# Optimization experiments

Hardware: AMD Instinct MI355X
Metric: run time of the kernel (lower is better)

## Reference

```python
import jax, jax.numpy as jnp
import numpy as np

T_IN, T_TGT, B = 192, 192, 128
XDIM, CH, H, Z, OUT = 64, 2, 512, 128, 64
XIN = XDIM * CH


def _gru_cell(h, x_proj, Whh, bhh):
    # torch GRU gate order: r, z, n
    hp = h @ Whh.T + bhh
    xr, xz, xn = jnp.split(x_proj, 3, axis=-1)
    hr, hz, hn = jnp.split(hp, 3, axis=-1)
    r = jax.nn.sigmoid(xr + hr)
    zg = jax.nn.sigmoid(xz + hz)
    n = jnp.tanh(xn + r * hn)
    return (1.0 - zg) * n + zg * h


def _run_gru(xs, h0, Wih, bih, Whh, bhh):
    xp = xs @ Wih.T + bih  # [T, B, 3H] precomputed input projections
    def step(h, xpt):
        h2 = _gru_cell(h, xpt, Whh, bhh)
        return h2, h2
    hT, outs = jax.lax.scan(step, h0, xp)
    return outs, hT


def setup_inputs() -> dict:
    key = jax.random.key(0)
    ks = jax.random.split(key, 40)
    p = lambda i, shape: jax.random.normal(ks[i], shape, jnp.float32) * 0.05
    inp = {
        "x": jax.random.normal(ks[0], (T_IN, B, XIN), jnp.float32),
        "target": jax.random.normal(ks[1], (T_TGT, B, XDIM), jnp.float32),
        "eps_z": jax.random.normal(ks[2], (2, B, Z), jnp.float32),
        "eps_y": jax.random.normal(ks[3], (T_TGT, B, OUT), jnp.float32),
        # phi_x MLP
        "W_phi1": p(4, (H, XIN)), "b_phi1": jnp.zeros((H,), jnp.float32),
        "W_phi2": p(5, (H, H)), "b_phi2": jnp.zeros((H,), jnp.float32),
        # encoder bidirectional GRU
        "Wih_ef": p(6, (3 * H, H)), "bih_ef": jnp.zeros((3 * H,), jnp.float32),
        "Whh_ef": p(7, (3 * H, H)), "bhh_ef": jnp.zeros((3 * H,), jnp.float32),
        "Wih_eb": p(8, (3 * H, H)), "bih_eb": jnp.zeros((3 * H,), jnp.float32),
        "Whh_eb": p(9, (3 * H, H)), "bhh_eb": jnp.zeros((3 * H,), jnp.float32),
        # latent heads
        "W_mean": p(10, (Z, H)), "b_mean": jnp.zeros((Z,), jnp.float32),
        "W_std": p(11, (Z, H)), "b_std": jnp.zeros((Z,), jnp.float32),
        # first decoder hidden
        "W_fh": p(12, (H, 2 * Z)), "b_fh": jnp.zeros((H,), jnp.float32),
        # decoder GRU, input size H + 2Z (order: [z_expanded, state])
        "Wih_d": p(13, (3 * H, 2 * Z + H)), "bih_d": jnp.zeros((3 * H,), jnp.float32),
        "Whh_d": p(14, (3 * H, H)), "bhh_d": jnp.zeros((3 * H,), jnp.float32),
        # decoder output heads
        "W_dm": p(15, (OUT, H)), "b_dm": jnp.zeros((OUT,), jnp.float32),
        "W_ds": p(16, (OUT, H)), "b_ds": jnp.zeros((OUT,), jnp.float32),
        "epoch": 0,
    }
    return inp


def reference(x, target, eps_z, eps_y,
              W_phi1, b_phi1, W_phi2, b_phi2,
              Wih_ef, bih_ef, Whh_ef, bhh_ef,
              Wih_eb, bih_eb, Whh_eb, bhh_eb,
              W_mean, b_mean, W_std, b_std,
              W_fh, b_fh, Wih_d, bih_d, Whh_d, bhh_d,
              W_dm, b_dm, W_ds, b_ds, epoch):
    Bsz, h_dim = x.shape[1], W_phi1.shape[0]
    two_z = W_fh.shape[1]
    # phi_x
    phi = jax.nn.relu(jax.nn.relu(x @ W_phi1.T + b_phi1) @ W_phi2.T + b_phi2)
    h0 = jnp.zeros((Bsz, h_dim), phi.dtype)
    # bidirectional encoder: final hidden of each direction
    _, hf = _run_gru(phi, h0, Wih_ef, bih_ef, Whh_ef, bhh_ef)
    _, hb = _run_gru(phi[::-1], h0, Wih_eb, bih_eb, Whh_eb, bhh_eb)
    enc_h = jnp.stack([hf, hb])  # [2, B, H]
    latent_mean = enc_h @ W_mean.T + b_mean
    latent_std = jax.nn.softplus(enc_h @ W_std.T + b_std)
    z = eps_z * latent_std + latent_mean  # [2, B, Z]
    z_exp = jnp.concatenate([z[0], z[1]], axis=1)  # [B, 2Z]
    dec_h0 = jnp.tanh(z_exp @ W_fh.T + b_fh)
    # decoder input = concat([z_exp, state]); split Wih_d columns accordingly
    W_z, W_s = Wih_d[:, :two_z], Wih_d[:, two_z:]
    z_proj = z_exp @ W_z.T + bih_d  # constant part of input projection

    def step(carry, eps_t):
        h, s = carry  # s is previous decoder_out (zeros at t=0)
        xp = z_proj + s @ W_s.T
        h2 = _gru_cell(h, xp, Whh_d, bhh_d)
        m = jax.nn.softplus(h2 @ W_dm.T + b_dm)
        st = jax.nn.softplus(h2 @ W_ds.T + b_ds)
        pred = eps_t * st + m
        return (h2, h2), (pred, m, st)

    s0 = jnp.zeros_like(dec_h0)
    _, (preds, means, stds) = jax.lax.scan(step, (dec_h0, s0), eps_y)
    return latent_mean, latent_std, z, preds, means, stds
```

## Files before the change

### kernel.cpp

```cpp
#include <hip/hip_runtime.h>
#include <stdint.h>

typedef __attribute__((ext_vector_type(4))) float    f32x4;
typedef __attribute__((ext_vector_type(8))) short    s16x8;
typedef __attribute__((ext_vector_type(4))) short    s16x4;
typedef __attribute__((ext_vector_type(4))) unsigned u32x4;
typedef __attribute__((ext_vector_type(8))) __bf16   bf16x8;

#define DEV __device__ __forceinline__

DEV float b2f(short h) {
  unsigned u = ((unsigned)(unsigned short)h) << 16;
  return __builtin_bit_cast(float, u);
}
DEV short f2b(float f) {
  unsigned u = __builtin_bit_cast(unsigned, f);
  u = (u + 0x7FFFu + ((u >> 16) & 1u)) >> 16;
  return (short)u;
}
DEV float fsig(float x) { return 1.0f / (1.0f + __expf(-x)); }
DEV float ftanh(float x) {
  x = fminf(fmaxf(x, -15.0f), 15.0f);
  float e = __expf(2.0f * x);
  return (e - 1.0f) / (e + 1.0f);
}
DEV float fsp(float x) { return (x > 20.0f) ? x : __logf(1.0f + __expf(x)); }

DEV f32x4 MFMA(s16x8 a, s16x8 b, f32x4 c) {
  return __builtin_amdgcn_mfma_f32_16x16x32_bf16(
      __builtin_bit_cast(bf16x8, a), __builtin_bit_cast(bf16x8, b), c, 0, 0, 0);
}
DEV void gload16(const void* g, void* l) {
  __builtin_amdgcn_global_load_lds(
      (const __attribute__((address_space(1))) unsigned*)g,
      (__attribute__((address_space(3))) unsigned*)l, 16, 0, 0);
}

DEV s16x8 ld16c(const short* p) {
  s16x8 r;
  asm volatile("global_load_dwordx4 %0, %1, off sc0 sc1" : "=v"(r) : "v"(p) : "memory");
  return r;
}
DEV void st8c(short* p, s16x4 v) {
  asm volatile("global_store_dwordx2 %0, %1, off sc0 sc1" :: "v"(p), "v"(v) : "memory");
}
DEV void stflagc(unsigned* p, unsigned v) {
  asm volatile("global_store_dword %0, %1, off sc0 sc1" :: "v"(p), "v"(v) : "memory");
}
DEV void poll8c(const unsigned* f, unsigned tgt) {
  unsigned gd = 0;
  for (;;) {
    u32x4 a, b;
    asm volatile("global_load_dwordx4 %0, %2, off sc0 sc1\n\t"
                 "global_load_dwordx4 %1, %2, off offset:16 sc0 sc1\n\t"
                 "s_waitcnt vmcnt(0)"
                 : "=v"(a), "=v"(b) : "v"(f) : "memory");
    unsigned m = a[0];
    m = a[1] < m ? a[1] : m; m = a[2] < m ? a[2] : m; m = a[3] < m ? a[3] : m;
    m = b[0] < m ? b[0] : m; m = b[1] < m ? b[1] : m;
    m = b[2] < m ? b[2] : m; m = b[3] < m ? b[3] : m;
    if (m >= tgt) return;
    if (++gd > (1u << 18)) return;
  }
}

__global__ void k_initf(unsigned* __restrict__ f) {
  stflagc(f + threadIdx.x * 2, 0u);
  stflagc(f + threadIdx.x * 2 + 1, 0u);
}

__global__ void k_f2b(const float* __restrict__ s, short* __restrict__ d, int n) {
  int i = (blockIdx.x * 256 + threadIdx.x) * 4;
  if (i >= n) return;
  float4 v = *(const float4*)(s + i);
  s16x4 o; o[0] = f2b(v.x); o[1] = f2b(v.y); o[2] = f2b(v.z); o[3] = f2b(v.w);
  *(s16x4*)(d + i) = o;
}
__global__ void k_f2bs(const float* __restrict__ s, short* __restrict__ d,
                       int cols, int sstr, int soff, int total) {
  int i = (blockIdx.x * 256 + threadIdx.x) * 4;
  if (i >= total) return;
  int r = i / cols, c = i - r * cols;
  float4 v = *(const float4*)(s + (size_t)r * sstr + soff + c);
  s16x4 o; o[0] = f2b(v.x); o[1] = f2b(v.y); o[2] = f2b(v.z); o[3] = f2b(v.w);
  *(s16x4*)(d + i) = o;
}
__global__ void k_build_dec(const float* __restrict__ Whh, const float* __restrict__ Wih,
                            short* __restrict__ out) {
  int i = (blockIdx.x * 256 + threadIdx.x) * 4;
  if (i >= 1048576) return;
  int r = i >> 9, c = i & 511;
  float4 v;
  if (r < 1024) {
    float4 a = *(const float4*)(Whh + (size_t)r * 512 + c);
    float4 b = *(const float4*)(Wih + (size_t)r * 768 + 256 + c);
    v = make_float4(a.x + b.x, a.y + b.y, a.z + b.z, a.w + b.w);
  } else if (r < 1536) {
    v = *(const float4*)(Wih + (size_t)r * 768 + 256 + c);
  } else {
    v = *(const float4*)(Whh + (size_t)(r - 512) * 512 + c);
  }
  s16x4 o; o[0] = f2b(v.x); o[1] = f2b(v.y); o[2] = f2b(v.z); o[3] = f2b(v.w);
  *(s16x4*)(out + i) = o;
}

template <int EPI>
__global__ __launch_bounds__(256) void kgemm(
    const short* __restrict__ A, const short* __restrict__ W,
    const float* __restrict__ bias, float* __restrict__ outF,
    short* __restrict__ outB, int M, int N, int K) {
  __shared__ short lA[8192];
  __shared__ short lB[8192];
  const int tid = threadIdx.x, lane = tid & 63, wid = tid >> 6;
  const int l15 = lane & 15, lq = lane >> 4;
  const int m0 = blockIdx.x * 128, n0 = blockIdx.y * 128;
  const int wr2 = wid >> 1, wc2 = wid & 1;
  const f32x4 vz = {0.f, 0.f, 0.f, 0.f};
  f32x4 acc[4][4];
#pragma unroll
  for (int i = 0; i < 4; ++i)
#pragma unroll
    for (int j = 0; j < 4; ++j) acc[i][j] = vz;
  const int Kb = K * 2;
  const int nkt = K >> 6;
  const int srow = lane >> 3, sk = (lane & 7) * 16;
  const char* gA = (const char*)A;
  const char* gW = (const char*)W;
  for (int kt = 0; kt < nkt; ++kt) {
    __syncthreads();
#pragma unroll
    for (int i = 0; i < 4; ++i) {
      const int c = wid * 4 + i;
      gload16(gA + (size_t)(m0 + c * 8 + srow) * Kb + kt * 128 + sk, (char*)lA + c * 1024);
      gload16(gW + (size_t)(n0 + c * 8 + srow) * Kb + kt * 128 + sk, (char*)lB + c * 1024);
    }
    __syncthreads();
#pragma unroll
    for (int kc = 0; kc < 2; ++kc) {
      s16x8 af[4], bf[4];
#pragma unroll
      for (int mt = 0; mt < 4; ++mt)
        af[mt] = *(const s16x8*)((const char*)lA + (wr2 * 64 + mt * 16 + l15) * 128 + kc * 64 + lq * 16);
#pragma unroll
      for (int nt = 0; nt < 4; ++nt)
        bf[nt] = *(const s16x8*)((const char*)lB + (wc2 * 64 + nt * 16 + l15) * 128 + kc * 64 + lq * 16);
#pragma unroll
      for (int mt = 0; mt < 4; ++mt)
#pragma unroll
        for (int nt = 0; nt < 4; ++nt)
          acc[mt][nt] = MFMA(af[mt], bf[nt], acc[mt][nt]);
    }
  }
#pragma unroll
  for (int mt = 0; mt < 4; ++mt) {
#pragma unroll
    for (int nt = 0; nt < 4; ++nt) {
      const int col = n0 + wc2 * 64 + nt * 16 + l15;
      const int rl = wr2 * 64 + mt * 16 + lq * 4;
      const int row = m0 + rl;
      const float bv = bias ? bias[col] : 0.f;
      if (EPI == 0) {
#pragma unroll
        for (int d = 0; d < 4; ++d) outF[(size_t)(row + d) * N + col] = acc[mt][nt][d] + bv;
      } else if (EPI == 1) {
#pragma unroll
        for (int d = 0; d < 4; ++d) {
          float v = acc[mt][nt][d] + bv;
          v = v > 0.f ? v : 0.f;
          outB[(size_t)(row + d) * N + col] = f2b(v);
        }
      } else if (EPI == 3) {
#pragma unroll
        for (int d = 0; d < 4; ++d) {
          float v = ftanh(acc[mt][nt][d] + bv);
          outF[(size_t)(row + d) * N + col] = v;
          outB[(size_t)(row + d) * N + col] = f2b(v);
        }
      } else {
#pragma unroll
        for (int d = 0; d < 4; ++d)
          outB[(size_t)(row + d) * N + col] = f2b(acc[mt][nt][d] + bv);
      }
    }
  }
}

DEV void enc_xp_load(const short* xp, int tt, int J0, int lq, int b,
                     short xv[3][4]) {
  const short* xr = xp + (size_t)(tt * 128 + b) * 1536;
#pragma unroll
  for (int g = 0; g < 3; ++g)
#pragma unroll
    for (int d = 0; d < 4; ++d)
      xv[g][d] = xr[g * 512 + J0 + lq * 4 + d];
}

__global__ __launch_bounds__(256, 1) void enc_scan(
    const short* __restrict__ xpTf, const short* __restrict__ xpTb,
    const short* __restrict__ Whf, const short* __restrict__ Whb,
    const float* __restrict__ bhf, const float* __restrict__ bhb,
    short* __restrict__ hB, short* __restrict__ ench,
    unsigned* __restrict__ flags) {
  const int tid = threadIdx.x, lane = tid & 63, wid = tid >> 6;
  const int l15 = lane & 15, lq = lane >> 4;
  const int w = blockIdx.x;
  const int gru = w >> 6, rr = w & 63, bg = rr >> 3, cw = rr & 7;
  const int J0 = (cw * 4 + wid) * 16, b0 = bg * 16;
  const int b = b0 + l15;
  const short* Wg = gru ? Whb : Whf;
  const float* bb = gru ? bhb : bhf;
  const short* xpT = gru ? xpTb : xpTf;
  short* hBg = hB + (size_t)gru * 131072;
  unsigned* gfl = flags + (gru * 8 + bg) * 16;
  const f32x4 vz = {0.f, 0.f, 0.f, 0.f};

  s16x8 wfr[3][16];
#pragma unroll
  for (int g = 0; g < 3; ++g) {
    const short* wrp = Wg + (size_t)(g * 512 + J0 + l15) * 512 + lq * 8;
#pragma unroll
    for (int kc = 0; kc < 16; ++kc) wfr[g][kc] = *(const s16x8*)(wrp + kc * 32);
  }
  float bi[3][4];
#pragma unroll
  for (int g = 0; g < 3; ++g)
#pragma unroll
    for (int d = 0; d < 4; ++d) bi[g][d] = bb[g * 512 + J0 + lq * 4 + d];
  float hpv[4];
#pragma unroll
  for (int d = 0; d < 4; ++d) hpv[d] = 0.f;

  short xpv[3][4];
  enc_xp_load(xpT, gru ? 191 : 0, J0, lq, b, xpv);
  const int chb = J0 + lq * 4;

  {
    s16x4 pk;
#pragma unroll
    for (int d = 0; d < 4; ++d) {
      float rg = fsig(b2f(xpv[0][d]) + bi[0][d]);
      float zg = fsig(b2f(xpv[1][d]) + bi[1][d]);
      float nn = ftanh(b2f(xpv[2][d]) + rg * bi[2][d]);
      float hv = (1.f - zg) * nn;
      hpv[d] = hv;
      pk[d] = f2b(hv);
    }
    st8c(hBg + (((size_t)((chb >> 3) * 128 + b)) << 3) + (chb & 7), pk);
    asm volatile("s_waitcnt vmcnt(0)" ::: "memory");
    __syncthreads();
    if (tid == 0) stflagc(gfl + cw, 1u);
    enc_xp_load(xpT, gru ? 190 : 1, J0, lq, b, xpv);
  }

  for (int t = 1; t < 192; ++t) {
    poll8c(gfl, (unsigned)t);
    s16x8 hb[16];
    const short* hsrc = hBg + ((t + 1) & 1) * 65536;
#pragma unroll
    for (int kc = 0; kc < 16; ++kc)
      hb[kc] = ld16c(hsrc + ((size_t)((kc * 4 + lq) * 128 + b) << 3));
    asm volatile("s_waitcnt vmcnt(0)" ::: "memory");
    __builtin_amdgcn_sched_barrier(0);
    f32x4 acc[3];
#pragma unroll
    for (int g = 0; g < 3; ++g) acc[g] = vz;
#pragma unroll
    for (int kc = 0; kc < 16; ++kc)
#pragma unroll
      for (int g = 0; g < 3; ++g) acc[g] = MFMA(wfr[g][kc], hb[kc], acc[g]);
    short* hdst = hBg + (t & 1) * 65536;
    s16x4 pk;
#pragma unroll
    for (int d = 0; d < 4; ++d) {
      float rg = fsig(b2f(xpv[0][d]) + acc[0][d] + bi[0][d]);
      float zg = fsig(b2f(xpv[1][d]) + acc[1][d] + bi[1][d]);
      float nn = ftanh(b2f(xpv[2][d]) + rg * (acc[2][d] + bi[2][d]));
      float hv = (1.f - zg) * nn + zg * hpv[d];
      hpv[d] = hv;
      pk[d] = f2b(hv);
    }
    st8c(hdst + (((size_t)((chb >> 3) * 128 + b)) << 3) + (chb & 7), pk);
    if (t == 191) *(s16x4*)(ench + (size_t)gru * 65536 + (size_t)b * 512 + chb) = pk;
    asm volatile("s_waitcnt vmcnt(0)" ::: "memory");
    __syncthreads();
    if (tid == 0) stflagc(gfl + cw, (unsigned)(t + 1));
    if (t < 191) {
      const int tp = t + 1;
      enc_xp_load(xpT, gru ? (191 - tp) : tp, J0, lq, b, xpv);
    }
  }
}

__global__ __launch_bounds__(256, 1) void dec_scan(
    const short* __restrict__ zpR, const short* __restrict__ Wd,
    const float* __restrict__ bhd, const float* __restrict__ pre0,
    const float* __restrict__ h0f, short* __restrict__ hB,
    short* __restrict__ Hs, unsigned* __restrict__ flags) {
  const int tid = threadIdx.x, lane = tid & 63, wid = tid >> 6;
  const int l15 = lane & 15, lq = lane >> 4;
  const int w = blockIdx.x;
  const int bg = w >> 3, m = w & 7;
  unsigned* gfl = flags + 256 + bg * 16;
  const int J0 = (m * 4 + wid) * 16, b0 = bg * 16;
  const int b = b0 + l15;
  const f32x4 vz = {0.f, 0.f, 0.f, 0.f};

  s16x8 wfr[4][16];
#pragma unroll
  for (int g = 0; g < 4; ++g) {
    const short* wrp = Wd + (size_t)(g * 512 + J0 + l15) * 512 + lq * 8;
#pragma unroll
    for (int kc = 0; kc < 16; ++kc) wfr[g][kc] = *(const s16x8*)(wrp + kc * 32);
  }
  float bi[3][4];
#pragma unroll
  for (int g = 0; g < 3; ++g)
#pragma unroll
    for (int d = 0; d < 4; ++d) bi[g][d] = bhd[g * 512 + J0 + lq * 4 + d];
  short zpv[3][4];
#pragma unroll
  for (int g = 0; g < 3; ++g)
#pragma unroll
    for (int d = 0; d < 4; ++d)
      zpv[g][d] = zpR[(size_t)b * 1536 + g * 512 + J0 + lq * 4 + d];
  float hpv[4];
#pragma unroll
  for (int d = 0; d < 4; ++d) hpv[d] = h0f[(size_t)b * 512 + J0 + lq * 4 + d];
  const int chb = J0 + lq * 4;

  {
    s16x4 pk;
#pragma unroll
    for (int d = 0; d < 4; ++d) {
      float p0 = pre0[(size_t)b * 1536 + 0 * 512 + J0 + lq * 4 + d];
      float p1 = pre0[(size_t)b * 1536 + 1 * 512 + J0 + lq * 4 + d];
      float p2 = pre0[(size_t)b * 1536 + 2 * 512 + J0 + lq * 4 + d];
      float rg = fsig(b2f(zpv[0][d]) + p0);
      float zg = fsig(b2f(zpv[1][d]) + p1);
      float nn = ftanh(b2f(zpv[2][d]) + rg * p2);
      float hv = (1.f - zg) * nn + zg * hpv[d];
      hpv[d] = hv;
      pk[d] = f2b(hv);
    }
    st8c(hB + (((size_t)((chb >> 3) * 128 + b)) << 3) + (chb & 7), pk);
    asm volatile("s_waitcnt vmcnt(0)" ::: "memory");
    __syncthreads();
    if (tid == 0) stflagc(gfl + m, 1u);
    *(s16x4*)(Hs + (size_t)b * 512 + chb) = pk;
  }

  for (int t = 1; t < 192; ++t) {
    poll8c(gfl, (unsigned)t);
    s16x8 hb[16];
    const short* hsrc = hB + ((t + 1) & 1) * 65536;
#pragma unroll
    for (int kc = 0; kc < 16; ++kc)
      hb[kc] = ld16c(hsrc + ((size_t)((kc * 4 + lq) * 128 + b) << 3));
    asm volatile("s_waitcnt vmcnt(0)" ::: "memory");
    __builtin_amdgcn_sched_barrier(0);
    f32x4 acc[4];
#pragma unroll
    for (int g = 0; g < 4; ++g) acc[g] = vz;
#pragma unroll
    for (int kc = 0; kc < 16; ++kc)
#pragma unroll
      for (int g = 0; g < 4; ++g) acc[g] = MFMA(wfr[g][kc], hb[kc], acc[g]);
    short* hdst = hB + (t & 1) * 65536;
    s16x4 pk;
#pragma unroll
    for (int d = 0; d < 4; ++d) {
      float rg = fsig(b2f(zpv[0][d]) + acc[0][d] + bi[0][d]);
      float zg = fsig(b2f(zpv[1][d]) + acc[1][d] + bi[1][d]);
      float nn = ftanh(b2f(zpv[2][d]) + acc[2][d] + rg * (acc[3][d] + bi[2][d]));
      float hv = (1.f - zg) * nn + zg * hpv[d];
      hpv[d] = hv;
      pk[d] = f2b(hv);
    }
    st8c(hdst + (((size_t)((chb >> 3) * 128 + b)) << 3) + (chb & 7), pk);
    asm volatile("s_waitcnt vmcnt(0)" ::: "memory");
    __syncthreads();
    if (tid == 0) stflagc(gfl + m, (unsigned)(t + 1));
    *(s16x4*)(Hs + (size_t)(t * 128 + b) * 512 + chb) = pk;
  }
}

__global__ void k_latent(const float* __restrict__ tmp, const float* __restrict__ b_mean,
                         const float* __restrict__ b_std, const float* __restrict__ eps_z,
                         float* __restrict__ out, short* __restrict__ zexp) {
  int i = blockIdx.x * 256 + threadIdx.x;
  if (i >= 32768) return;
  int c = i & 127, b = (i >> 7) & 127, g = i >> 14;
  float mp = tmp[(size_t)(g * 128 + b) * 256 + c] + b_mean[c];
  float sp = fsp(tmp[(size_t)(g * 128 + b) * 256 + 128 + c] + b_std[c]);
  float zv = eps_z[i] * sp + mp;
  out[i] = mp;
  out[32768 + i] = sp;
  out[65536 + i] = zv;
  zexp[b * 256 + g * 128 + c] = f2b(zv);
}

__global__ void k_preds(const float* __restrict__ tmp2, const float* __restrict__ b_dm,
                        const float* __restrict__ b_ds, const float* __restrict__ eps_y,
                        float* __restrict__ out) {
  int j = blockIdx.x * 256 + threadIdx.x;
  if (j >= 1572864) return;
  int c = j & 63;
  int row = j >> 6;
  float m = fsp(tmp2[(size_t)row * 128 + c] + b_dm[c]);
  float st = fsp(tmp2[(size_t)row * 128 + 64 + c] + b_ds[c]);
  out[98304 + j] = eps_y[j] * st + m;
  out[1671168 + j] = m;
  out[3244032 + j] = st;
}

extern "C" void kernel_launch(void* const* d_in, const int* in_sizes, int n_in,
                              void* d_out, int out_size, void* d_ws, size_t ws_size,
                              hipStream_t stream) {
  (void)in_sizes; (void)n_in; (void)out_size; (void)ws_size;
  const float* x      = (const float*)d_in[0];
  const float* eps_z  = (const float*)d_in[2];
  const float* eps_y  = (const float*)d_in[3];
  const float* W_phi1 = (const float*)d_in[4];
  const float* b_phi1 = (const float*)d_in[5];
  const float* W_phi2 = (const float*)d_in[6];
  const float* b_phi2 = (const float*)d_in[7];
  const float* Wih_ef = (const float*)d_in[8];
  const float* bih_ef = (const float*)d_in[9];
  const float* Whh_ef = (const float*)d_in[10];
  const float* bhh_ef = (const float*)d_in[11];
  const float* Wih_eb = (const float*)d_in[12];
  const float* bih_eb = (const float*)d_in[13];
  const float* Whh_eb = (const float*)d_in[14];
  const float* bhh_eb = (const float*)d_in[15];
  const float* W_mean = (const float*)d_in[16];
  const float* b_mean = (const float*)d_in[17];
  const float* W_std  = (const float*)d_in[18];
  const float* b_std  = (const float*)d_in[19];
  const float* W_fh   = (const float*)d_in[20];
  const float* b_fh   = (const float*)d_in[21];
  const float* Wih_d  = (const float*)d_in[22];
  const float* bih_d  = (const float*)d_in[23];
  const float* Whh_d  = (const float*)d_in[24];
  const float* bhh_d  = (const float*)d_in[25];
  const float* W_dm   = (const float*)d_in[26];
  const float* b_dm   = (const float*)d_in[27];
  const float* W_ds   = (const float*)d_in[28];
  const float* b_ds   = (const float*)d_in[29];
  float* out = (float*)d_out;
  char* ws = (char*)d_ws;

  short* x16  = (short*)(ws + 0);
  short* C1   = (short*)(ws + 6291456);
  short* Hs   = (short*)(ws + 0);
  short* phi  = (short*)(ws + 31457280);
  float* tmp2 = (float*)(ws + 31457280);
  short* xpf  = (short*)(ws + 56623104);
  short* xpb  = (short*)(ws + 132120576);
  short* w_dec = (short*)(ws + 56623104);
  float* pre0F = (float*)(ws + 58720256);
  short* h0b   = (short*)(ws + 59506688);
  char*  wb   = ws + 207618048;
  short* w_phi1_16 = (short*)(wb + 0);
  short* w_phi2_16 = (short*)(wb + 131072);
  short* w_ihef = (short*)(wb + 655360);
  short* w_hhef = (short*)(wb + 2228224);
  short* w_iheb = (short*)(wb + 3801088);
  short* w_hheb = (short*)(wb + 5373952);
  short* w_ms   = (short*)(wb + 6946816);
  short* w_fh   = (short*)(wb + 7208960);
  short* w_z    = (short*)(wb + 7471104);
  short* w_hhd  = (short*)(wb + 9830400);
  short* w_out  = (short*)(wb + 11403264);
  short* hBe   = (short*)(ws + 219152384);
  short* ench  = (short*)(ws + 219676672);
  float* tmpms = (float*)(ws + 219938816);
  short* zexp  = (short*)(ws + 220200960);
  float* h0f   = (float*)(ws + 220266496);
  short* hBd   = (short*)(ws + 220528640);
  short* zpR   = (short*)(ws + 220790784);
  unsigned* flags  = (unsigned*)(ws + 221184000);

  k_initf<<<1, 256, 0, stream>>>(flags);

  k_f2b<<<3072, 256, 0, stream>>>(x, x16, 3145728);
  k_f2b<<<64,   256, 0, stream>>>(W_phi1, w_phi1_16, 65536);
  k_f2b<<<256,  256, 0, stream>>>(W_phi2, w_phi2_16, 262144);
  k_f2b<<<768,  256, 0, stream>>>(Wih_ef, w_ihef, 786432);
  k_f2b<<<768,  256, 0, stream>>>(Whh_ef, w_hhef, 786432);
  k_f2b<<<768,  256, 0, stream>>>(Wih_eb, w_iheb, 786432);
  k_f2b<<<768,  256, 0, stream>>>(Whh_eb, w_hheb, 786432);
  k_f2b<<<64,   256, 0, stream>>>(W_mean, w_ms, 65536);
  k_f2b<<<64,   256, 0, stream>>>(W_std,  w_ms + 65536, 65536);
  k_f2b<<<128,  256, 0, stream>>>(W_fh, w_fh, 131072);
  k_f2b<<<768,  256, 0, stream>>>(Whh_d, w_hhd, 786432);
  k_f2b<<<32,   256, 0, stream>>>(W_dm, w_out, 32768);
  k_f2b<<<32,   256, 0, stream>>>(W_ds, w_out + 32768, 32768);
  k_f2bs<<<384, 256, 0, stream>>>(Wih_d, w_z, 256, 768, 0, 393216);

  kgemm<1><<<dim3(192, 4), 256, 0, stream>>>(x16, w_phi1_16, b_phi1, (float*)nullptr, C1, 24576, 512, 128);
  kgemm<1><<<dim3(192, 4), 256, 0, stream>>>(C1, w_phi2_16, b_phi2, (float*)nullptr, phi, 24576, 512, 512);
  kgemm<4><<<dim3(192, 12), 256, 0, stream>>>(phi, w_ihef, bih_ef, (float*)nullptr, xpf, 24576, 1536, 512);
  kgemm<4><<<dim3(192, 12), 256, 0, stream>>>(phi, w_iheb, bih_eb, (float*)nullptr, xpb, 24576, 1536, 512);
  enc_scan<<<128, 256, 0, stream>>>(xpf, xpb, w_hhef, w_hheb, bhh_ef, bhh_eb, hBe, ench, flags);
  k_build_dec<<<1024, 256, 0, stream>>>(Whh_d, Wih_d, w_dec);
  kgemm<0><<<dim3(2, 2), 256, 0, stream>>>(ench, w_ms, (const float*)nullptr, tmpms, (short*)nullptr, 256, 256, 512);
  k_latent<<<128, 256, 0, stream>>>(tmpms, b_mean, b_std, eps_z, out, zexp);
  kgemm<3><<<dim3(1, 4), 256, 0, stream>>>(zexp, w_fh, b_fh, h0f, h0b, 128, 512, 256);
  kgemm<4><<<dim3(1, 12), 256, 0, stream>>>(zexp, w_z, bih_d, (float*)nullptr, zpR, 128, 1536, 256);
  kgemm<0><<<dim3(1, 12), 256, 0, stream>>>(h0b, w_hhd, bhh_d, pre0F, (short*)nullptr, 128, 1536, 512);
  dec_scan<<<64, 256, 0, stream>>>(zpR, w_dec, bhh_d, pre0F, h0f, hBd, Hs, flags);
  kgemm<0><<<dim3(192, 1), 256, 0, stream>>>(Hs, w_out, (const float*)nullptr, tmp2, (short*)nullptr, 24576, 128, 512);
  k_preds<<<6144, 256, 0, stream>>>(tmp2, b_dm, b_ds, eps_y, out);
}
```

Baseline: 1.646 ms.

## Embed parity tag bits in hidden-state data to replace flag polling

The hidden-state values written each step now carry an epoch parity bit in the low mantissa bit of one bf16 element per 8-element chunk. Readers spin directly on the data until every chunk shows the expected parity, and fall back to the flag poll only after a bounded number of tries. This removes the separate flag round-trip (wait for flag, then load data) from the recurrent critical path. The cost is perturbing the low bit of some hidden values, repeated full loads while spinning, and an extra init kernel to seed the buffers.

```diff
diff --git a/kernel.cpp b/kernel.cpp
--- a/kernel.cpp
+++ b/kernel.cpp
@@ -67,6 +67,18 @@
 __global__ void k_initf(unsigned* __restrict__ f) {
   stflagc(f + threadIdx.x * 2, 0u);
   stflagc(f + threadIdx.x * 2 + 1, 0u);
+}
+__global__ void k_inith(short* __restrict__ hBe, short* __restrict__ hBd) {
+  int i = blockIdx.x * 256 + threadIdx.x;
+  s16x4 v; v[0] = 1; v[1] = 1; v[2] = 1; v[3] = 1;
+  if (i < 32768) {
+    st8c(hBe + (size_t)i * 8, v);
+    st8c(hBe + (size_t)i * 8 + 4, v);
+  } else if (i < 49152) {
+    int j = i - 32768;
+    st8c(hBd + (size_t)j * 8, v);
+    st8c(hBd + (size_t)j * 8 + 4, v);
+  }
 }
 
 __global__ void k_f2b(const float* __restrict__ s, short* __restrict__ d, int n) {
@@ -245,6 +257,7 @@
       hpv[d] = hv;
       pk[d] = f2b(hv);
     }
+    pk[0] = (short)(pk[0] & ~1);
     st8c(hBg + (((size_t)((chb >> 3) * 128 + b)) << 3) + (chb & 7), pk);
     asm volatile("s_waitcnt vmcnt(0)" ::: "memory");
     __syncthreads();
@@ -253,13 +266,29 @@
   }
 
   for (int t = 1; t < 192; ++t) {
-    poll8c(gfl, (unsigned)t);
+    const int E = ((t - 1) >> 1) & 1;
+    const int T = (t >> 1) & 1;
+    const short* hsrc = hBg + ((t + 1) & 1) * 65536;
     s16x8 hb[16];
-    const short* hsrc = hBg + ((t + 1) & 1) * 65536;
-#pragma unroll
-    for (int kc = 0; kc < 16; ++kc)
-      hb[kc] = ld16c(hsrc + ((size_t)((kc * 4 + lq) * 128 + b) << 3));
-    asm volatile("s_waitcnt vmcnt(0)" ::: "memory");
+    bool fresh = false;
+    for (int it = 0; it < 24; ++it) {
+#pragma unroll
+      for (int kc = 0; kc < 16; ++kc)
+        hb[kc] = ld16c(hsrc + ((size_t)((kc * 4 + lq) * 128 + b) << 3));
+      asm volatile("s_waitcnt vmcnt(0)" ::: "memory");
+      unsigned ok = 1u;
+#pragma unroll
+      for (int kc = 0; kc < 16; ++kc)
+        ok &= (unsigned)((hb[kc][0] & 1) == E) & (unsigned)((hb[kc][4] & 1) == E);
+      if (__all((int)ok)) { fresh = true; break; }
+    }
+    if (!fresh) {
+      poll8c(gfl, (unsigned)t);
+#pragma unroll
+      for (int kc = 0; kc < 16; ++kc)
+        hb[kc] = ld16c(hsrc + ((size_t)((kc * 4 + lq) * 128 + b) << 3));
+      asm volatile("s_waitcnt vmcnt(0)" ::: "memory");
+    }
     __builtin_amdgcn_sched_barrier(0);
     f32x4 acc[3];
 #pragma unroll
@@ -279,6 +308,7 @@
       hpv[d] = hv;
       pk[d] = f2b(hv);
     }
+    pk[0] = (short)((pk[0] & ~1) | T);
     st8c(hdst + (((size_t)((chb >> 3) * 128 + b)) << 3) + (chb & 7), pk);
     if (t == 191) *(s16x4*)(ench + (size_t)gru * 65536 + (size_t)b * 512 + chb) = pk;
     asm volatile("s_waitcnt vmcnt(0)" ::: "memory");
@@ -342,6 +372,7 @@
       hpv[d] = hv;
       pk[d] = f2b(hv);
     }
+    pk[0] = (short)(pk[0] & ~1);
     st8c(hB + (((size_t)((chb >> 3) * 128 + b)) << 3) + (chb & 7), pk);
     asm volatile("s_waitcnt vmcnt(0)" ::: "memory");
     __syncthreads();
@@ -350,13 +381,29 @@
   }
 
   for (int t = 1; t < 192; ++t) {
-    poll8c(gfl, (unsigned)t);
+    const int E = ((t - 1) >> 1) & 1;
+    const int T = (t >> 1) & 1;
+    const short* hsrc = hB + ((t + 1) & 1) * 65536;
     s16x8 hb[16];
-    const short* hsrc = hB + ((t + 1) & 1) * 65536;
-#pragma unroll
-    for (int kc = 0; kc < 16; ++kc)
-      hb[kc] = ld16c(hsrc + ((size_t)((kc * 4 + lq) * 128 + b) << 3));
-    asm volatile("s_waitcnt vmcnt(0)" ::: "memory");
+    bool fresh = false;
+    for (int it = 0; it < 24; ++it) {
+#pragma unroll
+      for (int kc = 0; kc < 16; ++kc)
+        hb[kc] = ld16c(hsrc + ((size_t)((kc * 4 + lq) * 128 + b) << 3));
+      asm volatile("s_waitcnt vmcnt(0)" ::: "memory");
+      unsigned ok = 1u;
+#pragma unroll
+      for (int kc = 0; kc < 16; ++kc)
+        ok &= (unsigned)((hb[kc][0] & 1) == E) & (unsigned)((hb[kc][4] & 1) == E);
+      if (__all((int)ok)) { fresh = true; break; }
+    }
+    if (!fresh) {
+      poll8c(gfl, (unsigned)t);
+#pragma unroll
+      for (int kc = 0; kc < 16; ++kc)
+        hb[kc] = ld16c(hsrc + ((size_t)((kc * 4 + lq) * 128 + b) << 3));
+      asm volatile("s_waitcnt vmcnt(0)" ::: "memory");
+    }
     __builtin_amdgcn_sched_barrier(0);
     f32x4 acc[4];
 #pragma unroll
@@ -376,6 +423,7 @@
       hpv[d] = hv;
       pk[d] = f2b(hv);
     }
+    pk[0] = (short)((pk[0] & ~1) | T);
     st8c(hdst + (((size_t)((chb >> 3) * 128 + b)) << 3) + (chb & 7), pk);
     asm volatile("s_waitcnt vmcnt(0)" ::: "memory");
     __syncthreads();
@@ -481,6 +529,7 @@
   unsigned* flags  = (unsigned*)(ws + 221184000);
 
   k_initf<<<1, 256, 0, stream>>>(flags);
+  k_inith<<<192, 256, 0, stream>>>(hBe, hBd);
 
   k_f2b<<<3072, 256, 0, stream>>>(x, x16, 3145728);
   k_f2b<<<64,   256, 0, stream>>>(W_phi1, w_phi1_16, 65536);
```

Measured after the change: 1.413 ms (median of 2 runs). -14.1%, faster.
